# Performance work log

Hardware: AMD Instinct MI355X
Metric: run time of the kernel (lower is better)

Reference implementation:

```python
import jax, jax.numpy as jnp
import numpy as np

B, L, D, S = 8, 512, 64, 8


def setup_inputs() -> dict:
    key = jax.random.key(0)
    ks = jax.random.split(key, 8)
    return {
        "lstm1": jax.random.normal(ks[0], (B, L, D), dtype=jnp.float32),
        "lstm2": jax.random.normal(ks[1], (B, L, D), dtype=jnp.float32),
        "W": jax.random.normal(ks[2], (S, D, D), dtype=jnp.float32) * 0.1,
        "V": jax.random.normal(ks[3], (S, 2 * D), dtype=jnp.float32) * 0.1,
        "b": jax.random.normal(ks[4], (S,), dtype=jnp.float32) * 0.1,
        "W_g": jax.random.normal(ks[5], (S, 2 * D), dtype=jnp.float32) * 0.1,
        "b_g": jax.random.normal(ks[6], (S,), dtype=jnp.float32) * 0.1,
        "u": jax.random.normal(ks[7], (1, S), dtype=jnp.float32) * 0.1,
    }


def reference(lstm1, lstm2, W, V, b, W_g, b_g, u):
    # lstm1/lstm2: (B, L, D). Pairwise slot (i, j) pairs lstm1[:, i] with lstm2[:, j].
    d = lstm1.shape[-1]
    # Bilinear tensor-network score: x1_i W_s x2_j -> (B, L, L, S)
    result_w = jnp.einsum('bid,sde,bje->bijs', lstm1, W, lstm2)
    # concat(x1_i, x2_j) @ V^T decomposed to avoid materializing (B,L,L,2D)
    v1 = jnp.einsum('bid,sd->bis', lstm1, V[:, :d])[:, :, None, :]   # (B,L,1,S)
    v2 = jnp.einsum('bjd,sd->bjs', lstm2, V[:, d:])[:, None, :, :]   # (B,1,L,S)
    result_v = v1 + v2                                               # (B,L,L,S)
    g1 = jnp.einsum('bid,sd->bis', lstm1, W_g[:, :d])[:, :, None, :]
    g2 = jnp.einsum('bjd,sd->bjs', lstm2, W_g[:, d:])[:, None, :, :]
    gate = jax.nn.sigmoid(g1 + g2 + b_g)                             # (B,L,L,S)
    result_final = gate * result_w + (1.0 - gate) * jax.nn.sigmoid(result_v) + b
    # Reduce slices with u (shape (1,S)) -> (B,L,L), then add singleton channel dim.
    out = jnp.einsum('bijs,ks->bijk', result_final, u)[..., 0]
    return out[:, None, :, :]  # (B, 1, L, L)
```

## Files before the change

### kernel.cpp

```cpp
#include <hip/hip_runtime.h>
#include <math.h>

typedef float f32x4 __attribute__((ext_vector_type(4)));
typedef short bf16x8 __attribute__((ext_vector_type(8)));

namespace {
constexpr int kB = 8, kL = 512, kD = 64, kS = 8;
constexpr int LP = 72;
constexpr size_t SCL_OFF = 0;
constexpr size_t WT_OFF  = (size_t)4 * 8 * 8 * 512 * 4;
constexpr size_t T_OFF   = WT_OFF + (size_t)8 * 64 * 64 * 2;
}

__device__ __forceinline__ unsigned short f2bf(float f) {
    unsigned u = __float_as_uint(f);
    u += 0x7FFFu + ((u >> 16) & 1u);
    return (unsigned short)(u >> 16);
}
__device__ __forceinline__ unsigned pk2(float lo, float hi) {
    return (unsigned)f2bf(lo) | ((unsigned)f2bf(hi) << 16);
}

__global__ __launch_bounds__(256) void grn_prep(
    const float* __restrict__ lstm1, const float* __restrict__ lstm2,
    const float* __restrict__ W, const float* __restrict__ V,
    const float* __restrict__ Wg, unsigned char* __restrict__ ws)
{
    float* scl = (float*)(ws + SCL_OFF);
    unsigned short* wt = (unsigned short*)(ws + WT_OFF);
    const int tid = threadIdx.x;
    if (blockIdx.x < 8) {
        const int s = blockIdx.x;
        __shared__ float wsm[64][68];
        const float* pw = W + s * 4096;
        const int row = tid >> 2, c0 = (tid & 3) * 16;
        #pragma unroll
        for (int q = 0; q < 4; q++)
            *(float4*)&wsm[row][c0 + q * 4] = *(const float4*)(pw + row * 64 + c0 + q * 4);
        __syncthreads();
        const int e = tid >> 2, d0 = (tid & 3) * 16;
        unsigned wd[8];
        #pragma unroll
        for (int q = 0; q < 8; q++)
            wd[q] = pk2(wsm[d0 + 2 * q][e], wsm[d0 + 2 * q + 1][e]);
        unsigned short* dst = wt + s * 4096 + e * 64 + d0;
        uint4 a = {wd[0], wd[1], wd[2], wd[3]};
        uint4 c = {wd[4], wd[5], wd[6], wd[7]};
        *(uint4*)(dst) = a;
        *(uint4*)(dst + 8) = c;
    } else {
        const int rb = blockIdx.x - 8;
        const int b = rb >> 3, r0 = (rb & 7) * 64;
        const int kind = tid & 3, row = r0 + (tid >> 2);
        const float* x = (kind < 2 ? lstm1 : lstm2) + ((size_t)b * kL + row) * kD;
        float xr[64];
        #pragma unroll
        for (int q = 0; q < 16; q++)
            *(float4*)&xr[q * 4] = *(const float4*)(x + q * 4);
        const float* vb = (kind & 1 ? Wg : V) + ((kind >> 1) ? kD : 0);
        #pragma unroll
        for (int s = 0; s < kS; s++) {
            const float* vec = vb + s * 2 * kD;
            float a = 0.f;
            #pragma unroll
            for (int q = 0; q < 16; q++) {
                const float4 vv = *(const float4*)(vec + q * 4);
                a = fmaf(vv.x, xr[q * 4 + 0], a);
                a = fmaf(vv.y, xr[q * 4 + 1], a);
                a = fmaf(vv.z, xr[q * 4 + 2], a);
                a = fmaf(vv.w, xr[q * 4 + 3], a);
            }
            scl[(((size_t)kind * 8 + b) * 8 + s) * 512 + row] = a;
        }
    }
}

__global__ __launch_bounds__(256) void grn_t(
    const float* __restrict__ lstm1, unsigned char* __restrict__ ws)
{
    const unsigned short* wt = (const unsigned short*)(ws + WT_OFF);
    unsigned short* T = (unsigned short*)(ws + T_OFF);
    const int s = blockIdx.x, it = blockIdx.y, b = blockIdx.z;
    __shared__ __align__(16) unsigned short x1t[64][LP];
    __shared__ __align__(16) unsigned short wtt[64][LP];
    const int tid = threadIdx.x;
    {
        const float* p = lstm1 + ((size_t)b * kL + it * 64) * kD;
        const int row = tid >> 2, c0 = (tid & 3) * 16;
        unsigned wd[8];
        #pragma unroll
        for (int q = 0; q < 4; q++) {
            const float4 v = *(const float4*)(p + row * 64 + c0 + q * 4);
            wd[q * 2 + 0] = pk2(v.x, v.y);
            wd[q * 2 + 1] = pk2(v.z, v.w);
        }
        uint4 a = {wd[0], wd[1], wd[2], wd[3]};
        uint4 c = {wd[4], wd[5], wd[6], wd[7]};
        *(uint4*)&x1t[row][c0] = a;
        *(uint4*)&x1t[row][c0 + 8] = c;
    }
    {
        const unsigned short* g = wt + s * 4096;
        #pragma unroll
        for (int k = 0; k < 2; k++) {
            const int q = tid + k * 256;
            *(uint4*)&wtt[q >> 3][(q & 7) * 8] = *(const uint4*)(g + q * 8);
        }
    }
    __syncthreads();
    const int lane = tid & 63, w = tid >> 6;
    const int wm = w >> 1, wn = w & 1;
    const int fr = lane & 15, fh = lane >> 4;
    bf16x8 A[2][2], Bf[2][2];
    #pragma unroll
    for (int mb = 0; mb < 2; mb++)
        #pragma unroll
        for (int kb = 0; kb < 2; kb++)
            A[mb][kb] = *(const bf16x8*)&x1t[wm * 32 + mb * 16 + fr][fh * 8 + kb * 32];
    #pragma unroll
    for (int nb = 0; nb < 2; nb++)
        #pragma unroll
        for (int kb = 0; kb < 2; kb++)
            Bf[nb][kb] = *(const bf16x8*)&wtt[wn * 32 + nb * 16 + fr][fh * 8 + kb * 32];
    unsigned short* tb = T + (((size_t)(b * 8 + s)) * 512 + it * 64) * 64;
    #pragma unroll
    for (int mb = 0; mb < 2; mb++)
        #pragma unroll
        for (int nb = 0; nb < 2; nb++) {
            f32x4 z = {0.f, 0.f, 0.f, 0.f};
            f32x4 acc = __builtin_amdgcn_mfma_f32_16x16x32_bf16(A[mb][0], Bf[nb][0], z, 0, 0, 0);
            acc = __builtin_amdgcn_mfma_f32_16x16x32_bf16(A[mb][1], Bf[nb][1], acc, 0, 0, 0);
            const int e = wn * 32 + nb * 16 + fr;
            #pragma unroll
            for (int r = 0; r < 4; r++) {
                const int i = wm * 32 + mb * 16 + fh * 4 + r;
                tb[i * 64 + e] = f2bf(acc[r]);
            }
        }
}

__global__ __launch_bounds__(256) void grn_mainm(
    const float* __restrict__ lstm2, const float* __restrict__ bS,
    const float* __restrict__ bg, const float* __restrict__ u,
    const unsigned char* __restrict__ ws, float* __restrict__ out)
{
    const float* sclw = (const float*)(ws + SCL_OFF);
    const unsigned short* T = (const unsigned short*)(ws + T_OFF);
    const int jt = blockIdx.x, it = blockIdx.y, b = blockIdx.z;
    __shared__ __align__(16) unsigned short x2t[64][LP];
    __shared__ __align__(16) unsigned short tst[64][LP];
    __shared__ float scl[4][kS][64];
    const int tid = threadIdx.x;
    {
        const float* p = lstm2 + ((size_t)b * kL + jt * 64) * kD;
        const int row = tid >> 2, c0 = (tid & 3) * 16;
        unsigned wd[8];
        #pragma unroll
        for (int q = 0; q < 4; q++) {
            const float4 v = *(const float4*)(p + row * 64 + c0 + q * 4);
            wd[q * 2 + 0] = pk2(v.x, v.y);
            wd[q * 2 + 1] = pk2(v.z, v.w);
        }
        uint4 a = {wd[0], wd[1], wd[2], wd[3]};
        uint4 c = {wd[4], wd[5], wd[6], wd[7]};
        *(uint4*)&x2t[row][c0] = a;
        *(uint4*)&x2t[row][c0 + 8] = c;
    }
    {
        const int p0 = tid * 8, kind = p0 >> 9, rem = p0 & 511, s = rem >> 6, cc = rem & 63;
        const int base = (kind < 2 ? it : jt) * 64;
        const float* g = sclw + (((size_t)kind * 8 + b) * 8 + s) * 512 + base + cc;
        *(float4*)&scl[kind][s][cc] = *(const float4*)g;
        *(float4*)&scl[kind][s][cc + 4] = *(const float4*)(g + 4);
    }
    __syncthreads();
    const int lane = tid & 63, w = tid >> 6;
    const int wm = w >> 1, wn = w & 1;
    const int fr = lane & 15, fh = lane >> 4;
    bf16x8 Bf[2][2];
    #pragma unroll
    for (int nb = 0; nb < 2; nb++)
        #pragma unroll
        for (int kb = 0; kb < 2; kb++)
            Bf[nb][kb] = *(const bf16x8*)&x2t[wn * 32 + nb * 16 + fr][fh * 8 + kb * 32];
    float bias_c = 0.f;
    #pragma unroll
    for (int s = 0; s < kS; s++) bias_c = fmaf(u[s], bS[s], bias_c);
    float oacc[2][2][4];
    #pragma unroll
    for (int mb = 0; mb < 2; mb++)
        #pragma unroll
        for (int nb = 0; nb < 2; nb++)
            #pragma unroll
            for (int r = 0; r < 4; r++) oacc[mb][nb][r] = bias_c;

    for (int s = 0; s < kS; s++) {
        __syncthreads();
        {
            const unsigned short* tb = T + (((size_t)(b * 8 + s)) * 512 + it * 64) * 64;
            #pragma unroll
            for (int k = 0; k < 2; k++) {
                const int q = tid + k * 256;
                *(uint4*)&tst[q >> 3][(q & 7) * 8] = *(const uint4*)(tb + q * 8);
            }
        }
        __syncthreads();
        bf16x8 A[2][2];
        #pragma unroll
        for (int mb = 0; mb < 2; mb++)
            #pragma unroll
            for (int kb = 0; kb < 2; kb++)
                A[mb][kb] = *(const bf16x8*)&tst[wm * 32 + mb * 16 + fr][fh * 8 + kb * 32];
        const float us = u[s], bgs = bg[s];
        #pragma unroll
        for (int mb = 0; mb < 2; mb++)
            #pragma unroll
            for (int nb = 0; nb < 2; nb++) {
                f32x4 z = {0.f, 0.f, 0.f, 0.f};
                f32x4 acc = __builtin_amdgcn_mfma_f32_16x16x32_bf16(A[mb][0], Bf[nb][0], z, 0, 0, 0);
                acc = __builtin_amdgcn_mfma_f32_16x16x32_bf16(A[mb][1], Bf[nb][1], acc, 0, 0, 0);
                const int jj = wn * 32 + nb * 16 + fr;
                const float v2 = scl[2][s][jj], g2 = scl[3][s][jj];
                #pragma unroll
                for (int r = 0; r < 4; r++) {
                    const int ii = wm * 32 + mb * 16 + fh * 4 + r;
                    const float v1 = scl[0][s][ii], g1 = scl[1][s][ii];
                    const float gate = 1.f / (1.f + __expf(-(g1 + g2 + bgs)));
                    const float sv = 1.f / (1.f + __expf(-(v1 + v2)));
                    const float res = fmaf(gate, acc[r] - sv, sv);
                    oacc[mb][nb][r] = fmaf(us, res, oacc[mb][nb][r]);
                }
            }
    }
    float* op = out + ((size_t)b * kL + it * 64) * kL + jt * 64;
    #pragma unroll
    for (int mb = 0; mb < 2; mb++)
        #pragma unroll
        for (int nb = 0; nb < 2; nb++)
            #pragma unroll
            for (int r = 0; r < 4; r++)
                op[(wm * 32 + mb * 16 + fh * 4 + r) * kL + wn * 32 + nb * 16 + fr]
                    = oacc[mb][nb][r];
}

extern "C" void kernel_launch(void* const* d_in, const int* in_sizes, int n_in,
                              void* d_out, int out_size, void* d_ws, size_t ws_size,
                              hipStream_t stream) {
    const float* lstm1 = (const float*)d_in[0];
    const float* lstm2 = (const float*)d_in[1];
    const float* W     = (const float*)d_in[2];
    const float* V     = (const float*)d_in[3];
    const float* bS    = (const float*)d_in[4];
    const float* Wg    = (const float*)d_in[5];
    const float* bg    = (const float*)d_in[6];
    const float* u     = (const float*)d_in[7];
    unsigned char* ws = (unsigned char*)d_ws;
    grn_prep<<<72, 256, 0, stream>>>(lstm1, lstm2, W, V, Wg, ws);
    grn_t<<<dim3(kS, kL / 64, kB), 256, 0, stream>>>(lstm1, ws);
    grn_mainm<<<dim3(kL / 64, kL / 64, kB), 256, 0, stream>>>(lstm2, bS, bg, u, ws, (float*)d_out);
}
```

Baseline: 114.7 us.

## Fuse bilinear T computation into main kernel with double-buffered W prefetch

Removes the separate grn_t kernel. Each main block now computes its own 64x64 tile of x1·W_s in-register with MFMA, stages it through LDS, and feeds it straight into the second MFMA stage. This drops one launch and the bf16 T round trip through global memory. The W_s slices are double-buffered in LDS and prefetched two slices ahead through registers, so the loop needs only one barrier per slice. The cost is that T is recomputed redundantly by every jt block, which adds MFMA work and LDS footprint per block.

```diff
diff --git a/kernel.cpp b/kernel.cpp
--- a/kernel.cpp
+++ b/kernel.cpp
@@ -9,7 +9,6 @@
 constexpr int LP = 72;
 constexpr size_t SCL_OFF = 0;
 constexpr size_t WT_OFF  = (size_t)4 * 8 * 8 * 512 * 4;
-constexpr size_t T_OFF   = WT_OFF + (size_t)8 * 64 * 64 * 2;
 }
 
 __device__ __forceinline__ unsigned short f2bf(float f) {
@@ -75,96 +74,44 @@
     }
 }
 
-__global__ __launch_bounds__(256) void grn_t(
-    const float* __restrict__ lstm1, unsigned char* __restrict__ ws)
-{
-    const unsigned short* wt = (const unsigned short*)(ws + WT_OFF);
-    unsigned short* T = (unsigned short*)(ws + T_OFF);
-    const int s = blockIdx.x, it = blockIdx.y, b = blockIdx.z;
-    __shared__ __align__(16) unsigned short x1t[64][LP];
-    __shared__ __align__(16) unsigned short wtt[64][LP];
-    const int tid = threadIdx.x;
-    {
-        const float* p = lstm1 + ((size_t)b * kL + it * 64) * kD;
-        const int row = tid >> 2, c0 = (tid & 3) * 16;
-        unsigned wd[8];
-        #pragma unroll
-        for (int q = 0; q < 4; q++) {
-            const float4 v = *(const float4*)(p + row * 64 + c0 + q * 4);
-            wd[q * 2 + 0] = pk2(v.x, v.y);
-            wd[q * 2 + 1] = pk2(v.z, v.w);
-        }
-        uint4 a = {wd[0], wd[1], wd[2], wd[3]};
-        uint4 c = {wd[4], wd[5], wd[6], wd[7]};
-        *(uint4*)&x1t[row][c0] = a;
-        *(uint4*)&x1t[row][c0 + 8] = c;
-    }
-    {
-        const unsigned short* g = wt + s * 4096;
-        #pragma unroll
-        for (int k = 0; k < 2; k++) {
-            const int q = tid + k * 256;
-            *(uint4*)&wtt[q >> 3][(q & 7) * 8] = *(const uint4*)(g + q * 8);
-        }
-    }
-    __syncthreads();
-    const int lane = tid & 63, w = tid >> 6;
-    const int wm = w >> 1, wn = w & 1;
-    const int fr = lane & 15, fh = lane >> 4;
-    bf16x8 A[2][2], Bf[2][2];
-    #pragma unroll
-    for (int mb = 0; mb < 2; mb++)
-        #pragma unroll
-        for (int kb = 0; kb < 2; kb++)
-            A[mb][kb] = *(const bf16x8*)&x1t[wm * 32 + mb * 16 + fr][fh * 8 + kb * 32];
-    #pragma unroll
-    for (int nb = 0; nb < 2; nb++)
-        #pragma unroll
-        for (int kb = 0; kb < 2; kb++)
-            Bf[nb][kb] = *(const bf16x8*)&wtt[wn * 32 + nb * 16 + fr][fh * 8 + kb * 32];
-    unsigned short* tb = T + (((size_t)(b * 8 + s)) * 512 + it * 64) * 64;
-    #pragma unroll
-    for (int mb = 0; mb < 2; mb++)
-        #pragma unroll
-        for (int nb = 0; nb < 2; nb++) {
-            f32x4 z = {0.f, 0.f, 0.f, 0.f};
-            f32x4 acc = __builtin_amdgcn_mfma_f32_16x16x32_bf16(A[mb][0], Bf[nb][0], z, 0, 0, 0);
-            acc = __builtin_amdgcn_mfma_f32_16x16x32_bf16(A[mb][1], Bf[nb][1], acc, 0, 0, 0);
-            const int e = wn * 32 + nb * 16 + fr;
-            #pragma unroll
-            for (int r = 0; r < 4; r++) {
-                const int i = wm * 32 + mb * 16 + fh * 4 + r;
-                tb[i * 64 + e] = f2bf(acc[r]);
-            }
-        }
-}
-
-__global__ __launch_bounds__(256) void grn_mainm(
-    const float* __restrict__ lstm2, const float* __restrict__ bS,
-    const float* __restrict__ bg, const float* __restrict__ u,
-    const unsigned char* __restrict__ ws, float* __restrict__ out)
+__global__ __launch_bounds__(256) void grn_fusedm(
+    const float* __restrict__ lstm1, const float* __restrict__ lstm2,
+    const float* __restrict__ bS, const float* __restrict__ bg,
+    const float* __restrict__ u, const unsigned char* __restrict__ ws,
+    float* __restrict__ out)
 {
     const float* sclw = (const float*)(ws + SCL_OFF);
-    const unsigned short* T = (const unsigned short*)(ws + T_OFF);
+    const unsigned short* wt = (const unsigned short*)(ws + WT_OFF);
     const int jt = blockIdx.x, it = blockIdx.y, b = blockIdx.z;
+    __shared__ __align__(16) unsigned short x1t[64][LP];
     __shared__ __align__(16) unsigned short x2t[64][LP];
-    __shared__ __align__(16) unsigned short tst[64][LP];
+    __shared__ __align__(16) unsigned short wbuf[2][64][LP];
+    __shared__ __align__(16) unsigned short ts[2][64][LP];
     __shared__ float scl[4][kS][64];
     const int tid = threadIdx.x;
     {
-        const float* p = lstm2 + ((size_t)b * kL + jt * 64) * kD;
+        const float* p1 = lstm1 + ((size_t)b * kL + it * 64) * kD;
+        const float* p2 = lstm2 + ((size_t)b * kL + jt * 64) * kD;
         const int row = tid >> 2, c0 = (tid & 3) * 16;
-        unsigned wd[8];
+        unsigned w1[8], w2[8];
         #pragma unroll
         for (int q = 0; q < 4; q++) {
-            const float4 v = *(const float4*)(p + row * 64 + c0 + q * 4);
-            wd[q * 2 + 0] = pk2(v.x, v.y);
-            wd[q * 2 + 1] = pk2(v.z, v.w);
-        }
-        uint4 a = {wd[0], wd[1], wd[2], wd[3]};
-        uint4 c = {wd[4], wd[5], wd[6], wd[7]};
-        *(uint4*)&x2t[row][c0] = a;
-        *(uint4*)&x2t[row][c0 + 8] = c;
+            const float4 a = *(const float4*)(p1 + row * 64 + c0 + q * 4);
+            const float4 c = *(const float4*)(p2 + row * 64 + c0 + q * 4);
+            w1[q * 2] = pk2(a.x, a.y); w1[q * 2 + 1] = pk2(a.z, a.w);
+            w2[q * 2] = pk2(c.x, c.y); w2[q * 2 + 1] = pk2(c.z, c.w);
+        }
+        uint4 a0 = {w1[0], w1[1], w1[2], w1[3]}, a1 = {w1[4], w1[5], w1[6], w1[7]};
+        uint4 c0v = {w2[0], w2[1], w2[2], w2[3]}, c1 = {w2[4], w2[5], w2[6], w2[7]};
+        *(uint4*)&x1t[row][c0] = a0; *(uint4*)&x1t[row][c0 + 8] = a1;
+        *(uint4*)&x2t[row][c0] = c0v; *(uint4*)&x2t[row][c0 + 8] = c1;
+    }
+    {
+        #pragma unroll
+        for (int k = 0; k < 2; k++) {
+            const int q = tid + k * 256;
+            *(uint4*)&wbuf[0][q >> 3][(q & 7) * 8] = *(const uint4*)(wt + q * 8);
+        }
     }
     {
         const int p0 = tid * 8, kind = p0 >> 9, rem = p0 & 511, s = rem >> 6, cc = rem & 63;
@@ -177,12 +124,20 @@
     const int lane = tid & 63, w = tid >> 6;
     const int wm = w >> 1, wn = w & 1;
     const int fr = lane & 15, fh = lane >> 4;
-    bf16x8 Bf[2][2];
+    bf16x8 A1[2][2], Bf[2][2];
+    #pragma unroll
+    for (int mb = 0; mb < 2; mb++)
+        #pragma unroll
+        for (int kb = 0; kb < 2; kb++)
+            A1[mb][kb] = *(const bf16x8*)&x1t[wm * 32 + mb * 16 + fr][fh * 8 + kb * 32];
     #pragma unroll
     for (int nb = 0; nb < 2; nb++)
         #pragma unroll
         for (int kb = 0; kb < 2; kb++)
             Bf[nb][kb] = *(const bf16x8*)&x2t[wn * 32 + nb * 16 + fr][fh * 8 + kb * 32];
+    uint4 wreg0 = *(const uint4*)(wt + 4096 + tid * 8);
+    uint4 wreg1 = *(const uint4*)(wt + 4096 + (tid + 256) * 8);
+
     float bias_c = 0.f;
     #pragma unroll
     for (int s = 0; s < kS; s++) bias_c = fmaf(u[s], bS[s], bias_c);
@@ -194,31 +149,46 @@
             #pragma unroll
             for (int r = 0; r < 4; r++) oacc[mb][nb][r] = bias_c;
 
+    #pragma unroll 1
     for (int s = 0; s < kS; s++) {
-        __syncthreads();
-        {
-            const unsigned short* tb = T + (((size_t)(b * 8 + s)) * 512 + it * 64) * 64;
-            #pragma unroll
-            for (int k = 0; k < 2; k++) {
-                const int q = tid + k * 256;
-                *(uint4*)&tst[q >> 3][(q & 7) * 8] = *(const uint4*)(tb + q * 8);
-            }
-        }
-        __syncthreads();
-        bf16x8 A[2][2];
-        #pragma unroll
-        for (int mb = 0; mb < 2; mb++)
+        const int p = s & 1;
+        bf16x8 WB[2][2];
+        #pragma unroll
+        for (int nb = 0; nb < 2; nb++)
             #pragma unroll
             for (int kb = 0; kb < 2; kb++)
-                A[mb][kb] = *(const bf16x8*)&tst[wm * 32 + mb * 16 + fr][fh * 8 + kb * 32];
-        const float us = u[s], bgs = bg[s];
+                WB[nb][kb] = *(const bf16x8*)&wbuf[p][wn * 32 + nb * 16 + fr][fh * 8 + kb * 32];
         #pragma unroll
         for (int mb = 0; mb < 2; mb++)
             #pragma unroll
             for (int nb = 0; nb < 2; nb++) {
                 f32x4 z = {0.f, 0.f, 0.f, 0.f};
-                f32x4 acc = __builtin_amdgcn_mfma_f32_16x16x32_bf16(A[mb][0], Bf[nb][0], z, 0, 0, 0);
-                acc = __builtin_amdgcn_mfma_f32_16x16x32_bf16(A[mb][1], Bf[nb][1], acc, 0, 0, 0);
+                f32x4 tacc = __builtin_amdgcn_mfma_f32_16x16x32_bf16(A1[mb][0], WB[nb][0], z, 0, 0, 0);
+                tacc = __builtin_amdgcn_mfma_f32_16x16x32_bf16(A1[mb][1], WB[nb][1], tacc, 0, 0, 0);
+                #pragma unroll
+                for (int r = 0; r < 4; r++)
+                    ts[p][wm * 32 + mb * 16 + fh * 4 + r][wn * 32 + nb * 16 + fr] = f2bf(tacc[r]);
+            }
+        *(uint4*)&wbuf[1 - p][tid >> 3][(tid & 7) * 8] = wreg0;
+        {
+            const int q = tid + 256;
+            *(uint4*)&wbuf[1 - p][q >> 3][(q & 7) * 8] = wreg1;
+        }
+        __syncthreads();
+        bf16x8 At[2][2];
+        #pragma unroll
+        for (int mb = 0; mb < 2; mb++)
+            #pragma unroll
+            for (int kb = 0; kb < 2; kb++)
+                At[mb][kb] = *(const bf16x8*)&ts[p][wm * 32 + mb * 16 + fr][fh * 8 + kb * 32];
+        const float us = u[s], bgs = bg[s];
+        #pragma unroll
+        for (int mb = 0; mb < 2; mb++)
+            #pragma unroll
+            for (int nb = 0; nb < 2; nb++) {
+                f32x4 z = {0.f, 0.f, 0.f, 0.f};
+                f32x4 acc = __builtin_amdgcn_mfma_f32_16x16x32_bf16(At[mb][0], Bf[nb][0], z, 0, 0, 0);
+                acc = __builtin_amdgcn_mfma_f32_16x16x32_bf16(At[mb][1], Bf[nb][1], acc, 0, 0, 0);
                 const int jj = wn * 32 + nb * 16 + fr;
                 const float v2 = scl[2][s][jj], g2 = scl[3][s][jj];
                 #pragma unroll
@@ -231,6 +201,9 @@
                     oacc[mb][nb][r] = fmaf(us, res, oacc[mb][nb][r]);
                 }
             }
+        const int sn = (s + 2) & 7;
+        wreg0 = *(const uint4*)(wt + sn * 4096 + tid * 8);
+        wreg1 = *(const uint4*)(wt + sn * 4096 + (tid + 256) * 8);
     }
     float* op = out + ((size_t)b * kL + it * 64) * kL + jt * 64;
     #pragma unroll
@@ -256,6 +229,6 @@
     const float* u     = (const float*)d_in[7];
     unsigned char* ws = (unsigned char*)d_ws;
     grn_prep<<<72, 256, 0, stream>>>(lstm1, lstm2, W, V, Wg, ws);
-    grn_t<<<dim3(kS, kL / 64, kB), 256, 0, stream>>>(lstm1, ws);
-    grn_mainm<<<dim3(kL / 64, kL / 64, kB), 256, 0, stream>>>(lstm2, bS, bg, u, ws, (float*)d_out);
-}
+    grn_fusedm<<<dim3(kL / 64, kL / 64, kB), 256, 0, stream>>>(
+        lstm1, lstm2, bS, bg, u, ws, (float*)d_out);
+}
```

Measured after the change: 110.7 us. 3.4% less time.
